# Optimization experiments

Measured on AMD Instinct MI355X. Metric: run time of the kernel, lower is better.

The kernel has to match this reference:

```python
import jax, jax.numpy as jnp
import numpy as np

N = 50000      # nodes
E = 800000     # edges
G = 512        # graphs in the batch
CAT = 32       # node category count
D = 128        # node_emb_dim == gnn_hidden_dim
H = 8          # gat heads
C = 16         # out channels per head (D // H)
EF = 8         # raw edge feature dim
EE = 64        # edge_emb_dim
L = 4          # gnn layers
NCLS = 10
NEG = jnp.float32(-1e9)
BN_EPS = 1e-5


def setup_inputs() -> dict:
    ks = jax.random.split(jax.random.key(0), 24)
    g = lambda k, shape, scale: jax.random.normal(ks[k], shape, jnp.float32) * scale
    return {
        "x_nodes": jax.random.randint(ks[0], (N,), 0, CAT),
        "edge_src": jax.random.randint(ks[1], (E,), 0, N),
        "edge_dst": jax.random.randint(ks[2], (E,), 0, N),
        "edge_attr": g(3, (E, EF), 1.0),
        "batch": jnp.sort(jax.random.randint(ks[4], (N,), 0, G)),
        "node_emb": g(5, (CAT, D), 1.0),
        "edge_W": g(6, (EF, EE), EF ** -0.5),
        "edge_b": jnp.zeros((EE,), jnp.float32),
        "Wl": g(7, (L, D, H * C), D ** -0.5),
        "bl": g(8, (L, H * C), 0.02),
        "Wr": g(9, (L, D, H * C), D ** -0.5),
        "br": g(10, (L, H * C), 0.02),
        "We": g(11, (L, EE, H * C), EE ** -0.5),
        "att": g(12, (L, H, C), C ** -0.5),
        "gbias": g(13, (L, H * C), 0.02),
        "bn_gamma": 1.0 + g(14, (L, H * C), 0.05),
        "bn_beta": g(15, (L, H * C), 0.02),
        "head_W": g(16, (D, NCLS), D ** -0.5),
        "head_b": jnp.zeros((NCLS,), jnp.float32),
    }


def reference(x_nodes, edge_src, edge_dst, edge_attr, batch, node_emb,
              edge_W, edge_b, Wl, bl, Wr, br, We, att, gbias,
              bn_gamma, bn_beta, head_W, head_b):
    x = node_emb[x_nodes]                                    # [N, D] node encoder
    eattr = edge_attr @ edge_W + edge_b                      # [E, EE] edge encoder

    # GATv2Conv add_self_loops: remove existing self loops (masking keeps static
    # shapes), then append one self loop per node with edge_attr = per-node mean
    # of incoming edge attrs (PyG fill_value='mean').
    mask = edge_src != edge_dst                              # [E]
    w = mask.astype(jnp.float32)[:, None]
    cnt = jnp.clip(jax.ops.segment_sum(w, edge_dst, N), 1.0)
    loop_attr = jax.ops.segment_sum(eattr * w, edge_dst, N) / cnt  # [N, EE]
    ea = jnp.concatenate([eattr, loop_attr], axis=0)         # [E+N, EE]
    idx = jnp.arange(N)
    s = jnp.concatenate([edge_src, idx])                     # [E+N]
    d = jnp.concatenate([edge_dst, idx])
    mall = jnp.concatenate([mask, jnp.ones((N,), bool)])

    for i in range(L):
        xl = (x @ Wl[i] + bl[i]).reshape(N, H, C)            # source transform
        xr = (x @ Wr[i] + br[i]).reshape(N, H, C)            # target transform
        ep = (ea @ We[i]).reshape(-1, H, C)                  # edge transform
        z = jax.nn.leaky_relu(xl[s] + xr[d] + ep, 0.2)       # [E+N, H, C]
        logits = jnp.einsum('ehc,hc->eh', z, att[i])         # [E+N, H]
        logits = jnp.where(mall[:, None], logits, NEG)
        # segment softmax over target node d (each node has a self loop -> nonempty)
        m = jax.ops.segment_max(logits, d, num_segments=N)   # [N, H]
        p = jnp.where(mall[:, None], jnp.exp(logits - m[d]), 0.0)
        alpha = p / jax.ops.segment_sum(p, d, N)[d]          # [E+N, H]
        h = jax.ops.segment_sum(alpha[..., None] * xl[s], d, N)  # [N, H, C]
        h = h.reshape(N, H * C) + gbias[i]
        # BatchNorm1d in eval mode with running stats (mean=0, var=1)
        h = bn_gamma[i] * h * (1.0 + BN_EPS) ** -0.5 + bn_beta[i]
        x = jax.nn.elu(h)                                    # dropout inactive (eval)

    # global mean pool over graphs
    gsum = jax.ops.segment_sum(x, batch, G)                  # [G, D]
    gcnt = jnp.clip(jax.ops.segment_sum(jnp.ones((N, 1), jnp.float32), batch, G), 1.0)
    return (gsum / gcnt) @ head_W + head_b                   # [G, NCLS]
```

## Files before the change

kernel.cpp:

```cpp
#include <hip/hip_runtime.h>
#include <hip/hip_fp16.h>
#include <math.h>

static constexpr int N  = 50000;
static constexpr int E  = 800000;
static constexpr int G  = 512;
static constexpr int D  = 128;
static constexpr int EF = 8;
static constexpr int EE = 64;
static constexpr int L  = 4;
static constexpr int NC = 10;

typedef _Float16 half8 __attribute__((ext_vector_type(8)));
typedef _Float16 h2v  __attribute__((ext_vector_type(2)));
typedef float f2v __attribute__((ext_vector_type(2)));
typedef float f32x4 __attribute__((ext_vector_type(4)));

union H4 { float4 f4; f32x4 v4; h2v h[4]; };

#if __has_builtin(__builtin_amdgcn_fdot2)
#define FDOT2(a, b, c) __builtin_amdgcn_fdot2((a), (b), (c), false)
#else
#define FDOT2(a, b, c) ((float)(a)[0]*(float)(b)[0] + (float)(a)[1]*(float)(b)[1] + (c))
#endif

__device__ __forceinline__ h2v pkrtz(float a, float b) {
    return (h2v)__builtin_amdgcn_cvt_pkrtz(a, b);
}
__device__ __forceinline__ h2v hmax2(h2v a, h2v b) {
#if __has_builtin(__builtin_elementwise_max)
    return __builtin_elementwise_max(a, b);
#else
    h2v r; r[0] = a[0] > b[0] ? a[0] : b[0]; r[1] = a[1] > b[1] ? a[1] : b[1]; return r;
#endif
}
__device__ __forceinline__ h2v hfma2(h2v a, h2v b, h2v c) {
#if __has_builtin(__builtin_elementwise_fma)
    return __builtin_elementwise_fma(a, b, c);
#else
    return a * b + c;
#endif
}
__device__ __forceinline__ float red8(float v) {
#if __has_builtin(__builtin_amdgcn_update_dpp)
    v += __builtin_bit_cast(float, __builtin_amdgcn_update_dpp(
            0, __builtin_bit_cast(int, v), 0xB1, 0xF, 0xF, true));
    v += __builtin_bit_cast(float, __builtin_amdgcn_update_dpp(
            0, __builtin_bit_cast(int, v), 0x4E, 0xF, 0xF, true));
    v += __builtin_bit_cast(float, __builtin_amdgcn_update_dpp(
            0, __builtin_bit_cast(int, v), 0x141, 0xF, 0xF, true));
#else
    v += __shfl_xor(v, 1); v += __shfl_xor(v, 2); v += __shfl_xor(v, 4);
#endif
    return v;
}

#define LOG2E 1.44269504088896340736f

static constexpr size_t pad64(size_t w){ return (w + 63) & ~size_t(63); }
static constexpr size_t O_CNT     = 0;
static constexpr size_t O_CURSOR  = O_CNT + pad64(N);
static constexpr size_t ZERO_END  = O_CURSOR + pad64(N);
static constexpr size_t O_CSROFF  = ZERO_END;
static constexpr size_t O_BSUM    = O_CSROFF + pad64(N+1);
static constexpr size_t O_CSRSRC  = O_BSUM + 64;
static constexpr size_t O_CSREA   = O_CSRSRC + pad64(E);
static constexpr size_t O_MH      = O_CSREA + pad64((size_t)E*4);
static constexpr size_t O_CFOLD   = O_MH + pad64((size_t)L*512);
static constexpr size_t O_LOOPM   = O_CFOLD + pad64(L*D);
static constexpr size_t O_SELFF   = O_LOOPM + pad64((size_t)N*4);
static constexpr size_t O_WFRAG   = O_SELFF + pad64(N);
static constexpr size_t O_XH      = O_WFRAG + pad64((size_t)L*16384);
static constexpr size_t O_XLH     = O_XH  + pad64((size_t)N*64);
static constexpr size_t O_XRH     = O_XLH + pad64((size_t)N*64);

static constexpr int PB_EMB  = (N * D) / 256;
static constexpr int PB_ZERO = ((int)ZERO_END + 255) / 256;
static constexpr int PB_WCVT = (L * 32768) / 256;
static constexpr int PB_FOLD = L;
static constexpr int PB_TOTAL = PB_EMB + PB_ZERO + PB_WCVT + PB_FOLD;

__global__ __launch_bounds__(256) void prep_kernel(
        const int* __restrict__ xn, const float* __restrict__ emb, __half* __restrict__ xh,
        float* __restrict__ zbase,
        const float* __restrict__ Wl, const float* __restrict__ Wr, _Float16* __restrict__ wfrag,
        const float* __restrict__ edge_W, const float* __restrict__ edge_b,
        const float* __restrict__ We, _Float16* __restrict__ Mh, float* __restrict__ cfold) {
    int bid = blockIdx.x, t = threadIdx.x;
    if (bid < PB_EMB) {
        int i = bid * 256 + t;
        int n = i >> 7, c = i & 127;
        xh[i] = __float2half_rn(emb[xn[n] * D + c]);
    } else if (bid < PB_EMB + PB_ZERO) {
        int i = (bid - PB_EMB) * 256 + t;
        if (i < (int)ZERO_END) zbase[i] = 0.0f;
    } else if (bid < PB_EMB + PB_ZERO + PB_WCVT) {
        int i = (bid - PB_EMB - PB_ZERO) * 256 + t;
        int j    = i & 7;
        int lane = (i >> 3) & 63;
        int nt   = (i >> 9) & 15;
        int kt   = (i >> 13) & 3;
        int l    = i >> 15;
        int k = kt * 32 + (lane >> 4) * 8 + j;
        int n = nt * 16 + (lane & 15);
        float v = (n < 128) ? Wl[((size_t)l * D + k) * D + n]
                            : Wr[((size_t)l * D + k) * D + (n - 128)];
        wfrag[i] = (_Float16)v;
    } else {
        int l = bid - PB_EMB - PB_ZERO - PB_WCVT;
        if (t >= 128) return;
        const float* Wel = We + (size_t)l * EE * D;
        for (int j = 0; j < EF; ++j) {
            float s = 0.f;
            for (int k = 0; k < EE; ++k) s += edge_W[j * EE + k] * Wel[k * D + t];
            Mh[((size_t)l * D + t) * 8 + j] = (_Float16)s;
        }
        float s = 0.f;
        for (int k = 0; k < EE; ++k) s += edge_b[k] * Wel[k * D + t];
        cfold[l * D + t] = s;
    }
}

__global__ void edge_cnt_kernel(const int* __restrict__ src, const int* __restrict__ dst,
                                int* __restrict__ cnt) {
    int e = blockIdx.x * blockDim.x + threadIdx.x;
    if (e >= E) return;
    if (src[e] != dst[e]) atomicAdd(&cnt[dst[e]], 1);
}

__global__ void scan1_kernel(const int* __restrict__ cnt, int* __restrict__ out ,
                             int* __restrict__ bsum) {
    __shared__ int lds[256];
    int b = blockIdx.x, t = threadIdx.x;
    int base = b * 1024 + t * 4;
    int v[4]; int s = 0;
    #pragma unroll
    for (int k = 0; k < 4; ++k) { int idx = base + k; v[k] = (idx < N) ? cnt[idx] : 0; s += v[k]; }
    lds[t] = s; __syncthreads();
    for (int off = 1; off < 256; off <<= 1) {
        int add = (t >= off) ? lds[t - off] : 0;
        __syncthreads();
        lds[t] += add;
        __syncthreads();
    }
    int run = (t > 0) ? lds[t - 1] : 0;
    #pragma unroll
    for (int k = 0; k < 4; ++k) { run += v[k]; int idx = base + k; if (idx < N) out[idx] = run; }
    if (t == 255) bsum[b] = lds[255];
}

__global__ void scan3_kernel(int* __restrict__ csr_off, const int* __restrict__ bsum) {
    int i = blockIdx.x * blockDim.x + threadIdx.x;
    if (i == 0) csr_off[0] = 0;
    if (i >= N) return;
    int b = i >> 10;
    int add = 0;
    for (int k = 0; k < b; ++k) add += bsum[k];
    csr_off[1 + i] += add;
}

__global__ void csr_fill_kernel(const int* __restrict__ src, const int* __restrict__ dst,
                                const float* __restrict__ eattr,
                                const int* __restrict__ csr_off, int* __restrict__ cursor,
                                int* __restrict__ csr_src, __half* __restrict__ csr_ea) {
    int e = blockIdx.x * blockDim.x + threadIdx.x;
    if (e >= E) return;
    int s = src[e], d = dst[e];
    if (s == d) return;
    int pos = csr_off[d] + atomicAdd(&cursor[d], 1);
    __builtin_nontemporal_store(s << 8, csr_src + pos);
    const float4* p = reinterpret_cast<const float4*>(eattr + (size_t)e * 8);
    float4 a = p[0], b = p[1];
    H4 h;
    h.h[0] = pkrtz(a.x, a.y); h.h[1] = pkrtz(a.z, a.w);
    h.h[2] = pkrtz(b.x, b.y); h.h[3] = pkrtz(b.z, b.w);
    __builtin_nontemporal_store(h.v4, reinterpret_cast<f32x4*>(csr_ea + (size_t)pos * 8));
}

__global__ void loopmean_kernel(const int* __restrict__ csr_off, const __half* __restrict__ csr_ea,
                                __half* __restrict__ loopm, float* __restrict__ selff) {
    int i = blockIdx.x * blockDim.x + threadIdx.x;
    int n = i >> 3, j = i & 7;
    if (n >= N) return;
    int beg = csr_off[n], end = csr_off[n + 1];
    float s = 0.f;
    for (int idx = beg; idx < end; ++idx) s += __half2float(csr_ea[(size_t)idx * 8 + j]);
    int c = end - beg;
    loopm[(size_t)n * 8 + j] = __float2half_rn(s / (float)(c > 1 ? c : 1));
    if (j == 0) selff[n] = (c > 0) ? 1.0f : 0.0f;
}

__global__ __launch_bounds__(256) void transform_kernel(
        const __half* __restrict__ xh, const _Float16* __restrict__ wfrag,
        const float* __restrict__ bl, const float* __restrict__ br,
        __half* __restrict__ xl_h, __half* __restrict__ xr_h) {
    int w = threadIdx.x >> 6, lane = threadIdx.x & 63;
    int quad = lane >> 4, r16 = lane & 15;
    int m0 = blockIdx.x * 16;
    const _Float16* xrow = reinterpret_cast<const _Float16*>(xh) + (size_t)(m0 + r16) * D + quad * 8;
    half8 a[4];
    #pragma unroll
    for (int kt = 0; kt < 4; ++kt) a[kt] = *reinterpret_cast<const half8*>(xrow + kt * 32);
    f32x4 acc[4];
    #pragma unroll
    for (int nt = 0; nt < 4; ++nt) { f32x4 z = {0.f, 0.f, 0.f, 0.f}; acc[nt] = z; }
    #pragma unroll
    for (int nt = 0; nt < 4; ++nt) {
        int ntile = w * 4 + nt;
        #pragma unroll
        for (int kt = 0; kt < 4; ++kt) {
            half8 b = *reinterpret_cast<const half8*>(
                wfrag + ((size_t)(kt * 16 + ntile) * 64 + lane) * 8);
            acc[nt] = __builtin_amdgcn_mfma_f32_16x16x32_f16(a[kt], b, acc[nt], 0, 0, 0);
        }
    }
    #pragma unroll
    for (int nt = 0; nt < 4; ++nt) {
        int n = (w * 4 + nt) * 16 + r16;
        float bias = (n < 128) ? bl[n] : br[n - 128];
        #pragma unroll
        for (int r = 0; r < 4; ++r) {
            int node = m0 + quad * 4 + r;
            float v = acc[nt][r] + bias;
            if (n < 128) xl_h[(size_t)node * D + n] = __float2half_rn(v);
            else         xr_h[(size_t)node * D + (n - 128)] = __float2half_rn(v);
        }
    }
}

__global__ __launch_bounds__(128) void aggregate_kernel(
        const __half* __restrict__ xl_h, const __half* __restrict__ xr_h,
        const __half* __restrict__ loopm, const float* __restrict__ selff,
        const int* __restrict__ csr_off, const int* __restrict__ csr_src,
        const __half* __restrict__ csr_ea,
        const _Float16* __restrict__ Mh, const float* __restrict__ cfold,
        const float* __restrict__ att, const float* __restrict__ gbias,
        const float* __restrict__ bn_gamma, const float* __restrict__ bn_beta,
        __half* __restrict__ xout) {
    int n = blockIdx.x * 2 + (threadIdx.x >> 6);
    int t = threadIdx.x & 63;
    int c0 = t * 2;
    const char* xlb = reinterpret_cast<const char*>(xl_h);
    int lb = t << 2;
    h2v attp = pkrtz(att[c0] * LOG2E, att[c0 + 1] * LOG2E);
    H4 m0u, m1u;
    m0u.f4 = *reinterpret_cast<const float4*>(Mh + (size_t)c0 * 8);
    m1u.f4 = *reinterpret_cast<const float4*>(Mh + (size_t)(c0 + 1) * 8);
    float cf0 = cfold[c0], cf1 = cfold[c0 + 1];
    h2v xrp = *reinterpret_cast<const h2v*>(xr_h + (size_t)n * D + c0);
    h2v xlp = *reinterpret_cast<const h2v*>(xl_h + (size_t)n * D + c0);
    const h2v c02 = {(_Float16)0.2f, (_Float16)0.2f};

    H4 lau;
    lau.f4 = *reinterpret_cast<const float4*>(loopm + (size_t)n * 8);
    float sf = selff[n];
    float ep0 = cf0 * sf, ep1 = cf1 * sf;
    #pragma unroll
    for (int k = 0; k < 4; ++k) { ep0 = FDOT2(lau.h[k], m0u.h[k], ep0); ep1 = FDOT2(lau.h[k], m1u.h[k], ep1); }
    {
        f2v xlf = __builtin_convertvector(xlp, f2v);
        f2v xrf = __builtin_convertvector(xrp, f2v);
        float z0 = xlf[0] + xrf[0] + ep0; z0 = fmaxf(z0, 0.2f * z0);
        float z1 = xlf[1] + xrf[1] + ep1; z1 = fmaxf(z1, 0.2f * z1);
        ep0 = FDOT2(pkrtz(z0, z1), attp, 0.0f);
    }
    float m = red8(ep0);
    float denom = 1.0f;
    h2v acc = xlp;

    int beg = csr_off[n], end = csr_off[n + 1];
    for (int base = beg; base < end; base += 64) {
        int cnt = end - base; if (cnt > 64) cnt = 64;
        int sreg = (t < cnt) ? csr_src[base + t] : 0;
        int i = 0;
        for (; i + 4 <= cnt; i += 4) {
            int o0 = __shfl(sreg, i),     o1 = __shfl(sreg, i + 1);
            int o2 = __shfl(sreg, i + 2), o3 = __shfl(sreg, i + 3);
            h2v g0 = *reinterpret_cast<const h2v*>(xlb + o0 + lb);
            h2v g1 = *reinterpret_cast<const h2v*>(xlb + o1 + lb);
            h2v g2 = *reinterpret_cast<const h2v*>(xlb + o2 + lb);
            h2v g3 = *reinterpret_cast<const h2v*>(xlb + o3 + lb);
            H4 e0u, e1u, e2u, e3u;
            e0u.f4 = *reinterpret_cast<const float4*>(csr_ea + (size_t)(base + i) * 8);
            e1u.f4 = *reinterpret_cast<const float4*>(csr_ea + (size_t)(base + i) * 8 + 8);
            e2u.f4 = *reinterpret_cast<const float4*>(csr_ea + (size_t)(base + i) * 8 + 16);
            e3u.f4 = *reinterpret_cast<const float4*>(csr_ea + (size_t)(base + i) * 8 + 24);
            float p00 = cf0, p01 = cf1, p10 = cf0, p11 = cf1;
            float p20 = cf0, p21 = cf1, p30 = cf0, p31 = cf1;
            #pragma unroll
            for (int k = 0; k < 4; ++k) {
                p00 = FDOT2(e0u.h[k], m0u.h[k], p00); p01 = FDOT2(e0u.h[k], m1u.h[k], p01);
                p10 = FDOT2(e1u.h[k], m0u.h[k], p10); p11 = FDOT2(e1u.h[k], m1u.h[k], p11);
                p20 = FDOT2(e2u.h[k], m0u.h[k], p20); p21 = FDOT2(e2u.h[k], m1u.h[k], p21);
                p30 = FDOT2(e3u.h[k], m0u.h[k], p30); p31 = FDOT2(e3u.h[k], m1u.h[k], p31);
            }
            h2v z0 = g0 + xrp + pkrtz(p00, p01);
            h2v z1 = g1 + xrp + pkrtz(p10, p11);
            h2v z2 = g2 + xrp + pkrtz(p20, p21);
            h2v z3 = g3 + xrp + pkrtz(p30, p31);
            z0 = hmax2(z0, z0 * c02); z1 = hmax2(z1, z1 * c02);
            z2 = hmax2(z2, z2 * c02); z3 = hmax2(z3, z3 * c02);
            float l0 = red8(FDOT2(z0, attp, 0.0f));
            float l1 = red8(FDOT2(z1, attp, 0.0f));
            float l2 = red8(FDOT2(z2, attp, 0.0f));
            float l3 = red8(FDOT2(z3, attp, 0.0f));
            float gm = fmaxf(fmaxf(l0, l1), fmaxf(l2, l3));
            float nm = fmaxf(m, gm);
            float wo = __builtin_amdgcn_exp2f(m - nm);
            float w0 = __builtin_amdgcn_exp2f(l0 - nm);
            float w1 = __builtin_amdgcn_exp2f(l1 - nm);
            float w2 = __builtin_amdgcn_exp2f(l2 - nm);
            float w3 = __builtin_amdgcn_exp2f(l3 - nm);
            denom = denom * wo + (w0 + w1) + (w2 + w3);
            acc = acc * pkrtz(wo, wo);
            acc = hfma2(pkrtz(w0, w0), g0, acc);
            acc = hfma2(pkrtz(w1, w1), g1, acc);
            acc = hfma2(pkrtz(w2, w2), g2, acc);
            acc = hfma2(pkrtz(w3, w3), g3, acc);
            m = nm;
        }
        for (; i < cnt; ++i) {
            int o0 = __shfl(sreg, i);
            h2v g0 = *reinterpret_cast<const h2v*>(xlb + o0 + lb);
            H4 e0u;
            e0u.f4 = *reinterpret_cast<const float4*>(csr_ea + (size_t)(base + i) * 8);
            float p00 = cf0, p01 = cf1;
            #pragma unroll
            for (int k = 0; k < 4; ++k) { p00 = FDOT2(e0u.h[k], m0u.h[k], p00); p01 = FDOT2(e0u.h[k], m1u.h[k], p01); }
            h2v z0 = g0 + xrp + pkrtz(p00, p01);
            z0 = hmax2(z0, z0 * c02);
            float l0 = red8(FDOT2(z0, attp, 0.0f));
            float nm = fmaxf(m, l0);
            float wo = __builtin_amdgcn_exp2f(m - nm);
            float w0 = __builtin_amdgcn_exp2f(l0 - nm);
            denom = denom * wo + w0;
            acc = acc * pkrtz(wo, wo);
            acc = hfma2(pkrtz(w0, w0), g0, acc);
            m = nm;
        }
    }
    f2v accf = __builtin_convertvector(acc, f2v);
    float inv = 1.0f / denom;
    float h0 = accf[0] * inv + gbias[c0];
    float h1 = accf[1] * inv + gbias[c0 + 1];
    h0 = bn_gamma[c0] * h0 * 0.999995000037499813f + bn_beta[c0];
    h1 = bn_gamma[c0 + 1] * h1 * 0.999995000037499813f + bn_beta[c0 + 1];
    h0 = h0 > 0.f ? h0 : (__expf(h0) - 1.0f);
    h1 = h1 > 0.f ? h1 : (__expf(h1) - 1.0f);
    *reinterpret_cast<__half2*>(xout + (size_t)n * D + c0) = __floats2half2_rn(h0, h1);
}

__device__ __forceinline__ int lower_bound_dev(const int* a, int n, int v) {
    int lo = 0, hi = n;
    while (lo < hi) { int mid = (lo + hi) >> 1; if (a[mid] < v) lo = mid + 1; else hi = mid; }
    return lo;
}

__global__ __launch_bounds__(128) void headpool_kernel(
        const __half* __restrict__ xh, const int* __restrict__ batch,
        const float* __restrict__ hW, const float* __restrict__ hb,
        float* __restrict__ out) {
    __shared__ float lds[128];
    int g = blockIdx.x, t = threadIdx.x;
    int lo = lower_bound_dev(batch, N, g);
    int hi = lower_bound_dev(batch, N, g + 1);
    float s = 0.f;
    #pragma unroll 4
    for (int i = lo; i < hi; ++i) s += __half2float(xh[(size_t)i * D + t]);
    int c = hi - lo;
    lds[t] = s / (float)(c > 1 ? c : 1);
    __syncthreads();
    if (t < NC) {
        float p = hb[t];
        #pragma unroll 8
        for (int cc = 0; cc < D; ++cc) p += lds[cc] * hW[cc * NC + t];
        out[g * NC + t] = p;
    }
}

extern "C" void kernel_launch(void* const* d_in, const int* in_sizes, int n_in,
                              void* d_out, int out_size, void* d_ws, size_t ws_size,
                              hipStream_t stream) {
    const int*   x_nodes   = (const int*)  d_in[0];
    const int*   edge_src  = (const int*)  d_in[1];
    const int*   edge_dst  = (const int*)  d_in[2];
    const float* edge_attr = (const float*)d_in[3];
    const int*   batch     = (const int*)  d_in[4];
    const float* node_emb  = (const float*)d_in[5];
    const float* edge_W    = (const float*)d_in[6];
    const float* edge_b    = (const float*)d_in[7];
    const float* Wl        = (const float*)d_in[8];
    const float* bl        = (const float*)d_in[9];
    const float* Wr        = (const float*)d_in[10];
    const float* br        = (const float*)d_in[11];
    const float* We        = (const float*)d_in[12];
    const float* att       = (const float*)d_in[13];
    const float* gbias     = (const float*)d_in[14];
    const float* bn_gamma  = (const float*)d_in[15];
    const float* bn_beta   = (const float*)d_in[16];
    const float* head_W    = (const float*)d_in[17];
    const float* head_b    = (const float*)d_in[18];
    float* out = (float*)d_out;

    float* ws = (float*)d_ws;
    int*    cnt      = (int*)(ws + O_CNT);
    int*    cursor   = (int*)(ws + O_CURSOR);
    int*    csr_off  = (int*)(ws + O_CSROFF);
    int*    bsum     = (int*)(ws + O_BSUM);
    int*    csr_src  = (int*)(ws + O_CSRSRC);
    __half* csr_ea   = (__half*)(ws + O_CSREA);
    _Float16* Mh     = (_Float16*)(ws + O_MH);
    float*  cfold    = ws + O_CFOLD;
    __half* loopm    = (__half*)(ws + O_LOOPM);
    float*  selff    = ws + O_SELFF;
    _Float16* wfrag  = (_Float16*)(ws + O_WFRAG);
    __half* xh   = (__half*)(ws + O_XH);
    __half* xl_h = (__half*)(ws + O_XLH);
    __half* xr_h = (__half*)(ws + O_XRH);

    prep_kernel<<<PB_TOTAL, 256, 0, stream>>>(x_nodes, node_emb, xh, ws,
                                              Wl, Wr, wfrag, edge_W, edge_b, We, Mh, cfold);
    edge_cnt_kernel<<<(E + 255) / 256, 256, 0, stream>>>(edge_src, edge_dst, cnt);
    {
        int nb = (N + 1023) / 1024;
        scan1_kernel<<<nb, 256, 0, stream>>>(cnt, csr_off + 1, bsum);
        scan3_kernel<<<(N + 255) / 256, 256, 0, stream>>>(csr_off, bsum);
    }
    csr_fill_kernel<<<(E + 255) / 256, 256, 0, stream>>>(edge_src, edge_dst, edge_attr,
                                                         csr_off, cursor, csr_src, csr_ea);
    loopmean_kernel<<<(N * 8 + 255) / 256, 256, 0, stream>>>(csr_off, csr_ea, loopm, selff);
    for (int l = 0; l < L; ++l) {
        transform_kernel<<<N / 16, 256, 0, stream>>>(
            xh, wfrag + (size_t)l * 32768, bl + l * D, br + l * D, xl_h, xr_h);
        aggregate_kernel<<<N / 2, 128, 0, stream>>>(
            xl_h, xr_h, loopm, selff, csr_off, csr_src, csr_ea,
            Mh + (size_t)l * D * 8, cfold + l * D, att + l * D, gbias + l * D,
            bn_gamma + l * D, bn_beta + l * D, xh);
    }
    headpool_kernel<<<G, 128, 0, stream>>>(xh, batch, head_W, head_b, out);

    (void)in_sizes; (void)n_in; (void)out_size; (void)ws_size;
}
```

Measured before the change: 567.7 us.

## Build CSR via per-edge rank array so CSR writes become coalesced

The edge-count pass now records each edge's atomic slot within its destination, so the second atomic cursor pass disappears. A rank-fill kernel scatters only edge indices into CSR order. A separate build kernel then gathers src and edge attributes per CSR position, which makes the large fp16 attribute writes coalesced instead of scattered. The cost is an extra kernel launch, two extra E-sized int arrays, and gathered reads of the edge attributes.

```diff
diff --git a/kernel.cpp b/kernel.cpp
--- a/kernel.cpp
+++ b/kernel.cpp
@@ -59,11 +59,12 @@
 
 static constexpr size_t pad64(size_t w){ return (w + 63) & ~size_t(63); }
 static constexpr size_t O_CNT     = 0;
-static constexpr size_t O_CURSOR  = O_CNT + pad64(N);
-static constexpr size_t ZERO_END  = O_CURSOR + pad64(N);
+static constexpr size_t ZERO_END  = pad64(N);
 static constexpr size_t O_CSROFF  = ZERO_END;
 static constexpr size_t O_BSUM    = O_CSROFF + pad64(N+1);
-static constexpr size_t O_CSRSRC  = O_BSUM + 64;
+static constexpr size_t O_MYOFF   = O_BSUM + 64;
+static constexpr size_t O_RANK    = O_MYOFF + pad64(E);
+static constexpr size_t O_CSRSRC  = O_RANK + pad64(E);
 static constexpr size_t O_CSREA   = O_CSRSRC + pad64(E);
 static constexpr size_t O_MH      = O_CSREA + pad64((size_t)E*4);
 static constexpr size_t O_CFOLD   = O_MH + pad64((size_t)L*512);
@@ -122,10 +123,11 @@
 }
 
 __global__ void edge_cnt_kernel(const int* __restrict__ src, const int* __restrict__ dst,
-                                int* __restrict__ cnt) {
+                                int* __restrict__ cnt, int* __restrict__ myoff) {
     int e = blockIdx.x * blockDim.x + threadIdx.x;
     if (e >= E) return;
-    if (src[e] != dst[e]) atomicAdd(&cnt[dst[e]], 1);
+    int s = src[e], d = dst[e];
+    myoff[e] = (s == d) ? -1 : atomicAdd(&cnt[d], 1);
 }
 
 __global__ void scan1_kernel(const int* __restrict__ cnt, int* __restrict__ out ,
@@ -159,22 +161,28 @@
     csr_off[1 + i] += add;
 }
 
-__global__ void csr_fill_kernel(const int* __restrict__ src, const int* __restrict__ dst,
-                                const float* __restrict__ eattr,
-                                const int* __restrict__ csr_off, int* __restrict__ cursor,
-                                int* __restrict__ csr_src, __half* __restrict__ csr_ea) {
+__global__ void rank_fill_kernel(const int* __restrict__ dst, const int* __restrict__ csr_off,
+                                 const int* __restrict__ myoff, int* __restrict__ rank) {
     int e = blockIdx.x * blockDim.x + threadIdx.x;
     if (e >= E) return;
-    int s = src[e], d = dst[e];
-    if (s == d) return;
-    int pos = csr_off[d] + atomicAdd(&cursor[d], 1);
-    __builtin_nontemporal_store(s << 8, csr_src + pos);
+    int mo = myoff[e];
+    if (mo < 0) return;
+    rank[csr_off[dst[e]] + mo] = e;
+}
+
+__global__ void csr_build_kernel(const int* __restrict__ rank, const int* __restrict__ src,
+                                 const float* __restrict__ eattr, const int* __restrict__ total,
+                                 int* __restrict__ csr_src, __half* __restrict__ csr_ea) {
+    int pos = blockIdx.x * blockDim.x + threadIdx.x;
+    if (pos >= *total) return;
+    int e = rank[pos];
+    csr_src[pos] = src[e] << 8;
     const float4* p = reinterpret_cast<const float4*>(eattr + (size_t)e * 8);
     float4 a = p[0], b = p[1];
     H4 h;
     h.h[0] = pkrtz(a.x, a.y); h.h[1] = pkrtz(a.z, a.w);
     h.h[2] = pkrtz(b.x, b.y); h.h[3] = pkrtz(b.z, b.w);
-    __builtin_nontemporal_store(h.v4, reinterpret_cast<f32x4*>(csr_ea + (size_t)pos * 8));
+    *reinterpret_cast<f32x4*>(csr_ea + (size_t)pos * 8) = h.v4;
 }
 
 __global__ void loopmean_kernel(const int* __restrict__ csr_off, const __half* __restrict__ csr_ea,
@@ -404,9 +412,10 @@
 
     float* ws = (float*)d_ws;
     int*    cnt      = (int*)(ws + O_CNT);
-    int*    cursor   = (int*)(ws + O_CURSOR);
     int*    csr_off  = (int*)(ws + O_CSROFF);
     int*    bsum     = (int*)(ws + O_BSUM);
+    int*    myoff    = (int*)(ws + O_MYOFF);
+    int*    rank     = (int*)(ws + O_RANK);
     int*    csr_src  = (int*)(ws + O_CSRSRC);
     __half* csr_ea   = (__half*)(ws + O_CSREA);
     _Float16* Mh     = (_Float16*)(ws + O_MH);
@@ -420,14 +429,15 @@
 
     prep_kernel<<<PB_TOTAL, 256, 0, stream>>>(x_nodes, node_emb, xh, ws,
                                               Wl, Wr, wfrag, edge_W, edge_b, We, Mh, cfold);
-    edge_cnt_kernel<<<(E + 255) / 256, 256, 0, stream>>>(edge_src, edge_dst, cnt);
+    edge_cnt_kernel<<<(E + 255) / 256, 256, 0, stream>>>(edge_src, edge_dst, cnt, myoff);
     {
         int nb = (N + 1023) / 1024;
         scan1_kernel<<<nb, 256, 0, stream>>>(cnt, csr_off + 1, bsum);
         scan3_kernel<<<(N + 255) / 256, 256, 0, stream>>>(csr_off, bsum);
     }
-    csr_fill_kernel<<<(E + 255) / 256, 256, 0, stream>>>(edge_src, edge_dst, edge_attr,
-                                                         csr_off, cursor, csr_src, csr_ea);
+    rank_fill_kernel<<<(E + 255) / 256, 256, 0, stream>>>(edge_dst, csr_off, myoff, rank);
+    csr_build_kernel<<<(E + 255) / 256, 256, 0, stream>>>(rank, edge_src, edge_attr,
+                                                          csr_off + N, csr_src, csr_ea);
     loopmean_kernel<<<(N * 8 + 255) / 256, 256, 0, stream>>>(csr_off, csr_ea, loopm, selff);
     for (int l = 0; l < L; ++l) {
         transform_kernel<<<N / 16, 256, 0, stream>>>(
```

New measurement: 538.1 us. 5.2% less time.
